# Kernel tuning notes

Hardware: AMD Instinct MI355X
Metric: run time of the kernel (lower is better)

The kernel has to match this reference:

```python
import jax, jax.numpy as jnp
import numpy as np

HEADS = 12
DIM_HEAD = 64
SCALE = DIM_HEAD ** -0.5


def _attn(q, k, v):
    # q: [B, I, D], k/v: [B, J, D]
    sim = jnp.einsum('bid,bjd->bij', q, k)
    a = jax.nn.softmax(sim, axis=-1)
    out = jnp.einsum('bij,bjd->bid', a, v)
    return out, a


def setup_inputs() -> dict:
    key = jax.random.key(0)
    k1, k2, k3 = jax.random.split(key, 3)
    B, F, N, DIM = 8, 8, 196, 768
    x = jax.random.normal(k1, (B, 1 + F * N, DIM), dtype=jnp.float32)
    W_qkv = jax.random.normal(k2, (DIM, 3 * HEADS * DIM_HEAD), dtype=jnp.float32) * (DIM ** -0.5)
    W_out = jax.random.normal(k3, (HEADS * DIM_HEAD, DIM), dtype=jnp.float32) * ((HEADS * DIM_HEAD) ** -0.5)
    b_out = jnp.zeros((DIM,), dtype=jnp.float32)
    return {"x": x, "W_qkv": W_qkv, "W_out": W_out, "b_out": b_out, "f": F}


def reference(x, W_qkv, W_out, b_out, f):
    b, n_tot, dim = x.shape
    h, d = HEADS, DIM_HEAD
    qkv = x @ W_qkv                              # [b, n, 3*h*d]
    q, k, v = jnp.split(qkv, 3, axis=-1)
    # 'b n (h d) -> (b h) n d'
    def to_bh(t):
        return t.reshape(b, n_tot, h, d).transpose(0, 2, 1, 3).reshape(b * h, n_tot, d)
    q, k, v = map(to_bh, (q, k, v))
    q = q * SCALE
    cls_q, q_ = q[:, :1], q[:, 1:]
    cls_k, k_ = k[:, :1], k[:, 1:]
    cls_v, v_ = v[:, :1], v[:, 1:]
    # cls token attends over full sequence
    cls_out, cls_attn = _attn(cls_q, k, v)       # [(b h), 1, d], [(b h), 1, n_tot]
    # spatial attention: 'b (f n) d -> (b f) n d'
    bh = b * h
    n = (n_tot - 1) // f
    def to_bf(t):
        return t.reshape(bh, f, n, d).reshape(bh * f, n, d)
    q_, k_, v_ = map(to_bf, (q_, k_, v_))
    r = f  # q_.shape[0] // cls_k.shape[0]
    # repeat 'b () d -> (b r) () d'
    cls_k_r = jnp.repeat(cls_k, r, axis=0)       # [(bh f), 1, d]
    cls_v_r = jnp.repeat(cls_v, r, axis=0)
    k_ = jnp.concatenate((cls_k_r, k_), axis=1)  # [(bh f), 1+n, d]
    v_ = jnp.concatenate((cls_v_r, v_), axis=1)
    out, _ = _attn(q_, k_, v_)                   # [(bh f), n, d]
    # '(b f) n d -> b (f n) d' (with b := bh)
    out = out.reshape(bh, f * n, d)
    out = jnp.concatenate((cls_out, out), axis=1)  # [(b h), n_tot, d]
    # '(b h) n d -> b n (h d)'
    out = out.reshape(b, h, n_tot, d).transpose(0, 2, 1, 3).reshape(b, n_tot, h * d)
    return out @ W_out + b_out, cls_attn
```

## Files before the change

### kernel.cpp

```cpp
#include <hip/hip_runtime.h>

typedef unsigned short u16;
typedef unsigned int u32;
typedef __attribute__((ext_vector_type(8))) short s16x8;
typedef __attribute__((ext_vector_type(4))) float f32x4;
typedef __attribute__((ext_vector_type(4))) u32 u32x4;
typedef __attribute__((ext_vector_type(4))) float fvec4;

#define DEV static __device__ __forceinline__

typedef __attribute__((address_space(1))) unsigned char ga_u8;
typedef __attribute__((address_space(3))) unsigned char la_u8;

DEV u16 f2bf(float f){
  u32 u = __builtin_bit_cast(u32, f);
  u32 r = (u + 0x7FFFu + ((u >> 16) & 1u)) >> 16;
  return (u16)r;
}
DEV float bf2f(u16 v){
  u32 x = ((u32)v) << 16;
  return __builtin_bit_cast(float, x);
}
DEV f32x4 mfma16(s16x8 a, s16x8 b, f32x4 c){
  return __builtin_amdgcn_mfma_f32_16x16x32_bf16(a, b, c, 0, 0, 0);
}
DEV s16x8 ld16B(const u16* p){
  return __builtin_bit_cast(s16x8, *(const u32x4*)p);
}
DEV u32 cvt_pk_bf16(float lo, float hi){
  u32 r;
  asm volatile("v_cvt_pk_bf16_f32 %0, %1, %2" : "=v"(r) : "v"(lo), "v"(hi));
  return r;
}
DEV void gload16(const void* g, void* l){
  __builtin_amdgcn_global_load_lds((const ga_u8*)g, (la_u8*)l, 16, 0, 0);
}
DEV int xcd_chunk(int bid, int nwg){
  int q = nwg >> 3, r = nwg & 7;
  int xcd = bid & 7, lin = bid >> 3;
  return (xcd < r ? xcd*(q+1) : r*(q+1) + (xcd-r)*q) + lin;
}

#define BARRIER() __builtin_amdgcn_s_barrier()
#define VMC4()    asm volatile("s_waitcnt vmcnt(4)" ::: "memory")
#define VMC0()    asm volatile("s_waitcnt vmcnt(0)" ::: "memory")


__global__ __launch_bounds__(256) void k_prep(const float* __restrict__ x, u16* __restrict__ xb,
                                              const float* __restrict__ Wqkv, u16* __restrict__ wqkvT,
                                              const float* __restrict__ Wout, u16* __restrict__ woutT){
  __shared__ float tile[32][33];
  int b = blockIdx.x, tid = threadIdx.x;
  if (b < 2048){
    const int n4 = 12552*768/4;
    for (int i = b*256 + tid; i < n4; i += 2048*256){
      fvec4 v = ((const fvec4*)x)[i];
      u32 lo = (u32)f2bf(v[0]) | ((u32)f2bf(v[1]) << 16);
      u32 hi = (u32)f2bf(v[2]) | ((u32)f2bf(v[3]) << 16);
      ((u32*)xb)[2*i]   = lo;
      ((u32*)xb)[2*i+1] = hi;
    }
    return;
  }
  const float* W; u16* WT; int K, N, bn, bk;
  if (b < 2048 + 1728){
    int bb = b - 2048; W = Wqkv; WT = wqkvT; K = 768; N = 2304;
    bn = (bb % 72) * 32; bk = (bb / 72) * 32;
  } else {
    int bb = b - 3776; W = Wout; WT = woutT; K = 768; N = 768;
    bn = (bb % 24) * 32; bk = (bb / 24) * 32;
  }
  int tx = tid & 31, ty = tid >> 5;
  #pragma unroll
  for (int r = ty; r < 32; r += 8)
    tile[r][tx] = W[(size_t)(bk + r)*N + bn + tx];
  __syncthreads();
  #pragma unroll
  for (int r = ty; r < 32; r += 8)
    WT[(size_t)(bn + r)*K + bk + tx] = f2bf(tile[tx][r]);
}

__global__ __launch_bounds__(512, 2) void gemm_qkv(const u16* __restrict__ A, const u16* __restrict__ BT,
                                                   u16* __restrict__ qout, u16* __restrict__ kout, u16* __restrict__ vout){
  __shared__ u16 sA[2][2][128*64];
  __shared__ u16 sB[2][2][128*64];
  const int M = 12552;
  const int NWG = 50*9;
  int logical = xcd_chunk(blockIdx.x, NWG);
  int bxi = logical % 9, byi = logical / 9;
  int bm = byi * 256, bn = bxi * 256;

  int tid = threadIdx.x;
  int w = tid >> 6, l = tid & 63, l15 = l & 15, l4 = l >> 4;
  int wm = w >> 2, wn = w & 3;
  int swz = (l15 & 7) << 3;

  f32x4 acc[8][4];
  #pragma unroll
  for (int a=0;a<8;a++)
    #pragma unroll
    for (int b=0;b<4;b++) acc[a][b] = (f32x4){0.f,0.f,0.f,0.f};

  auto stageA = [&](int dbuf, int h, int kt){
    #pragma unroll
    for (int i=0;i<2;i++){
      int ci = i*512 + tid;
      int cs = ci ^ ((ci>>3)&7);
      int r = cs>>3, cc = (cs&7)*8;
      int gr = bm + h*128 + r; if (gr >= M) gr = M-1;
      gload16(A + (size_t)gr*768 + kt*64 + cc, &sA[dbuf][h][(i*512 + (w<<6))*8]);
    }
  };
  auto stageB = [&](int dbuf, int h, int kt){
    #pragma unroll
    for (int i=0;i<2;i++){
      int ci = i*512 + tid;
      int cs = ci ^ ((ci>>3)&7);
      int r = cs>>3, cc = (cs&7)*8;
      gload16(BT + (size_t)(bn + h*128 + r)*768 + kt*64 + cc, &sB[dbuf][h][(i*512 + (w<<6))*8]);
    }
  };

  s16x8 af[4][2], bf[4][2];
  #define LDA_(d, mi, kk) ld16B(&sA[d][wm][(((mi)*16 + l15)*64 + (kk)*32 + l4*8) ^ swz])
  #define LDB_(d, ni, kk) ld16B(&sB[d][(wn*64 + (ni)*16 + l15)>>7][((((wn*64 + (ni)*16 + l15)&127))*64 + (kk)*32 + l4*8) ^ swz])
  #define QUAD(MH, NH) do{ \
    __builtin_amdgcn_s_setprio(1); \
    _Pragma("unroll") \
    for (int j=0;j<4;j++){ \
      _Pragma("unroll") \
      for (int n=0;n<2;n++){ \
        acc[(MH)*4+j][(NH)*2+n] = mfma16(af[j][0], bf[(NH)*2+n][0], acc[(MH)*4+j][(NH)*2+n]); \
        acc[(MH)*4+j][(NH)*2+n] = mfma16(af[j][1], bf[(NH)*2+n][1], acc[(MH)*4+j][(NH)*2+n]); \
      } } \
    __builtin_amdgcn_s_setprio(0); }while(0)

  stageA(0,0,0); stageA(0,1,0); stageB(0,0,0); stageB(0,1,0);
  stageA(1,0,1); stageA(1,1,1);
  VMC4();
  BARRIER();

  #pragma unroll 1
  for (int it = 0; it < 6; ++it){
    int kt1 = 2*it + 1;
    bool full = (it < 5);
    #pragma unroll
    for (int j=0;j<4;j++){ af[j][0]=LDA_(0,j,0); af[j][1]=LDA_(0,j,1); }
    #pragma unroll
    for (int n=0;n<2;n++){ bf[n][0]=LDB_(0,n,0); bf[n][1]=LDB_(0,n,1); }
    stageB(1, 0, kt1);
    BARRIER();
    QUAD(0,0);
    BARRIER();
    #pragma unroll
    for (int n=2;n<4;n++){ bf[n][0]=LDB_(0,n,0); bf[n][1]=LDB_(0,n,1); }
    stageB(1, 1, kt1);
    BARRIER();
    QUAD(0,1);
    BARRIER();
    #pragma unroll
    for (int j=0;j<4;j++){ af[j][0]=LDA_(0,4+j,0); af[j][1]=LDA_(0,4+j,1); }
    if (full){ stageA(0, 0, kt1+1); stageA(0, 1, kt1+1); }
    BARRIER();
    QUAD(1,0); QUAD(1,1);
    if (full) { VMC4(); } else { VMC0(); }
    BARRIER();
    #pragma unroll
    for (int j=0;j<4;j++){ af[j][0]=LDA_(1,j,0); af[j][1]=LDA_(1,j,1); }
    #pragma unroll
    for (int n=0;n<2;n++){ bf[n][0]=LDB_(1,n,0); bf[n][1]=LDB_(1,n,1); }
    if (full) stageB(0, 0, kt1+1);
    BARRIER();
    QUAD(0,0);
    BARRIER();
    #pragma unroll
    for (int n=2;n<4;n++){ bf[n][0]=LDB_(1,n,0); bf[n][1]=LDB_(1,n,1); }
    if (full) stageB(0, 1, kt1+1);
    BARRIER();
    QUAD(0,1);
    BARRIER();
    #pragma unroll
    for (int j=0;j<4;j++){ af[j][0]=LDA_(1,4+j,0); af[j][1]=LDA_(1,4+j,1); }
    if (full){ stageA(1, 0, kt1+2); stageA(1, 1, kt1+2); }
    BARRIER();
    QUAD(1,0); QUAD(1,1);
    if (full) VMC4();
    BARRIER();
  }
  #undef LDA_
  #undef LDB_
  #undef QUAD

  int which = bn / 768;
  int h = ((bn - which*768) >> 6) + wn;
  u16* dst  = (which==0) ? qout : ((which==1) ? kout : vout);
  float scale = (which==0) ? 0.125f : 1.f;
  #pragma unroll
  for (int mi=0; mi<8; mi++){
    #pragma unroll
    for (int r=0; r<4; r++){
      int m = bm + wm*128 + mi*16 + l4*4 + r;
      if (m >= M) continue;
      int b = m / 1569, t = m - b*1569;
      u16* drow = dst + ((size_t)(b*12 + h)*1569 + t)*64 + l15;
      #pragma unroll
      for (int n=0; n<4; n++)
        drow[n*16] = f2bf(acc[mi][n][r] * scale);
    }
  }
}

__global__ __launch_bounds__(256, 2) void k_attn(const u16* __restrict__ qb, const u16* __restrict__ kb,
                                                 const u16* __restrict__ vb, u16* __restrict__ ob,
                                                 float* __restrict__ simw, float* __restrict__ bsum,
                                                 float* __restrict__ pvp){
  __shared__ u16 Vt[64][232];
  __shared__ float rs_lds[4][64];

  int blk = blockIdx.x, tid = threadIdx.x;

  if (blk >= 768){
    int bb = blk - 768;
    int c = bb % 7, g = bb / 7;
    __shared__ float qv[64];
    __shared__ float e_lds[256];
    __shared__ float red[256];
    if (tid < 64) qv[tid] = bf2f(qb[(size_t)g*1569*64 + tid]);
    __syncthreads();
    int j = c*256 + tid;
    float e = 0.f;
    if (j < 1569){
      const u16* kr = kb + ((size_t)g*1569 + j)*64;
      float a = 0.f;
      #pragma unroll
      for (int d0 = 0; d0 < 64; d0 += 8){
        u32x4 u = *(const u32x4*)(kr + d0);
        const u16* us = (const u16*)&u;
        #pragma unroll
        for (int i=0;i<8;i++) a += qv[d0+i]*bf2f(us[i]);
      }
      e = __expf(a - 8.f);
      simw[(size_t)g*1569 + j] = e;
    }
    e_lds[tid] = e;
    red[tid] = e; __syncthreads();
    for (int st=128; st>0; st>>=1){ if (tid<st) red[tid] += red[tid+st]; __syncthreads(); }
    if (tid == 0) bsum[g*8 + c] = red[0];
    int d = tid & 63, kk = tid >> 6;
    float a = 0.f;
    for (int jj = kk; jj < 256; jj += 4){
      int jg = c*256 + jj;
      if (jg < 1569) a += e_lds[jj] * bf2f(vb[((size_t)g*1569+jg)*64 + d]);
    }
    red[tid] = a; __syncthreads();
    if (tid < 64) pvp[((size_t)g*7 + c)*64 + tid] = red[tid]+red[tid+64]+red[tid+128]+red[tid+192];
    return;
  }

  int g = blk;
  int bh = g >> 3, fi = g & 7;
  int w = tid >> 6, l = tid & 63;
  int l15 = l & 15, l4 = l >> 4;

  const u16* qg = qb + ((size_t)bh*1569 + 1 + fi*196)*64;
  const u16* kg = kb + (size_t)bh*1569*64;
  const u16* vg = vb + (size_t)bh*1569*64;

  {
    int jj = tid >> 3, c = (tid & 7)*8, k8 = tid & 7;
    #pragma unroll
    for (int base = 0; base < 224; base += 32){
      int j = base + jj;
      u32x4 vv = {0,0,0,0};
      if (j < 197){
        int t = (j == 0) ? 0 : (1 + fi*196 + j - 1);
        vv = *(const u32x4*)(vg + (size_t)t*64 + c);
      }
      int jl = j & 31;
      int col = (j & ~31) + ((jl>>2)&3)*8 + (jl>>4)*4 + (jl&3);
      const u16* vp = (const u16*)&vv;
      #pragma unroll
      for (int i=0;i<8;i++){ int ii = (i + k8) & 7; Vt[c+ii][col] = vp[ii]; }
    }
  }

  s16x8 qf[4][2];
  #pragma unroll
  for (int mt=0; mt<4; mt++){
    int row = w*64 + mt*16 + l15;
    #pragma unroll
    for (int kk=0; kk<2; kk++){
      if (row < 196) qf[mt][kk] = ld16B(qg + (size_t)row*64 + kk*32 + l4*8);
      else { u32x4 z = {0,0,0,0}; qf[mt][kk] = __builtin_bit_cast(s16x8, z); }
    }
  }

  f32x4 acc[4][4];
  float rsum[4] = {0.f, 0.f, 0.f, 0.f};
  #pragma unroll
  for (int a=0;a<4;a++)
    #pragma unroll
    for (int b=0;b<4;b++) acc[a][b] = (f32x4){0.f,0.f,0.f,0.f};

  __syncthreads();

  #pragma unroll
  for (int ck = 0; ck < 7; ck++){
    int r0 = ck*32 + l15;
    int r1 = r0 + 16;
    int c0 = (r0 < 197 ? r0 : 196);
    int c1 = (r1 < 197 ? r1 : 196);
    int t0 = (r0 == 0) ? 0 : (1 + fi*196 + c0 - 1);
    int t1 = 1 + fi*196 + c1 - 1;
    s16x8 kf0[2], kf1[2];
    #pragma unroll
    for (int kk=0; kk<2; kk++){
      kf0[kk] = ld16B(kg + (size_t)t0*64 + kk*32 + l4*8);
      kf1[kk] = ld16B(kg + (size_t)t1*64 + kk*32 + l4*8);
    }
    s16x8 vf[4];
    #pragma unroll
    for (int ntd=0; ntd<4; ntd++) vf[ntd] = ld16B(&Vt[ntd*16 + l15][ck*32 + l4*8]);
    int kbase = ck*32 + l4*4;

    #pragma unroll
    for (int mt=0; mt<4; mt++){
      __builtin_amdgcn_s_setprio(1);
      f32x4 s0 = (f32x4){0.f,0.f,0.f,0.f}, s1 = (f32x4){0.f,0.f,0.f,0.f};
      s0 = mfma16(kf0[0], qf[mt][0], s0);
      s0 = mfma16(kf0[1], qf[mt][1], s0);
      s1 = mfma16(kf1[0], qf[mt][0], s1);
      s1 = mfma16(kf1[1], qf[mt][1], s1);
      __builtin_amdgcn_s_setprio(0);
      float p[8];
      #pragma unroll
      for (int r=0; r<4; r++){
        p[r]   = (kbase + r      < 197) ? __expf(s0[r] - 8.f) : 0.f;
        p[4+r] = (kbase + 16 + r < 197) ? __expf(s1[r] - 8.f) : 0.f;
      }
      rsum[mt] += ((p[0]+p[1])+(p[2]+p[3])) + ((p[4]+p[5])+(p[6]+p[7]));
      u32x4 pw;
      pw[0] = cvt_pk_bf16(p[0], p[1]);
      pw[1] = cvt_pk_bf16(p[2], p[3]);
      pw[2] = cvt_pk_bf16(p[4], p[5]);
      pw[3] = cvt_pk_bf16(p[6], p[7]);
      s16x8 pa = __builtin_bit_cast(s16x8, pw);
      __builtin_amdgcn_s_setprio(1);
      #pragma unroll
      for (int ntd=0; ntd<4; ntd++)
        acc[mt][ntd] = mfma16(pa, vf[ntd], acc[mt][ntd]);
      __builtin_amdgcn_s_setprio(0);
    }
  }

  #pragma unroll
  for (int mt=0; mt<4; mt++){
    float rs = rsum[mt];
    rs += __shfl_xor(rs, 16);
    rs += __shfl_xor(rs, 32);
    rs_lds[w][mt*16 + l15] = rs;
  }

  u16* og = ob + ((size_t)bh*1569 + 1 + fi*196)*64;
  #pragma unroll
  for (int mt=0; mt<4; mt++){
    #pragma unroll
    for (int r=0; r<4; r++){
      int row = w*64 + mt*16 + l4*4 + r;
      if (row < 196){
        float inv = 1.f / rs_lds[w][mt*16 + l4*4 + r];
        #pragma unroll
        for (int ntd=0; ntd<4; ntd++)
          og[(size_t)row*64 + ntd*16 + l15] = f2bf(acc[mt][ntd][r] * inv);
      }
    }
  }
}

__global__ __launch_bounds__(256) void cls_b(const float* __restrict__ simw, const float* __restrict__ bsum,
                                             const float* __restrict__ pvp, float* __restrict__ attn,
                                             u16* __restrict__ ob){
  int g = blockIdx.x, tid = threadIdx.x;
  float s = 0.f;
  #pragma unroll
  for (int c=0;c<7;c++) s += bsum[g*8+c];
  float inv = 1.f/s;
  for (int j = tid; j < 1569; j += 256)
    attn[(size_t)g*1569+j] = simw[(size_t)g*1569+j]*inv;
  if (tid < 64){
    float a = 0.f;
    #pragma unroll
    for (int c=0;c<7;c++) a += pvp[((size_t)g*7+c)*64 + tid];
    ob[(size_t)g*1569*64 + tid] = f2bf(a*inv);
  }
}

__global__ __launch_bounds__(512, 2) void gemm_out(const u16* __restrict__ AO, const u16* __restrict__ BT,
                                                   const float* __restrict__ bias, float* __restrict__ C){
  __shared__ u16 sA[2][2][128*64];
  __shared__ u16 sB[2][2][128*64];
  const int M = 12552;
  const int NWG = 50*3;
  int logical = xcd_chunk(blockIdx.x, NWG);
  int bxi = logical % 3, byi = logical / 3;
  int bm = byi * 256, bn = bxi * 256;

  int tid = threadIdx.x;
  int w = tid >> 6, l = tid & 63, l15 = l & 15, l4 = l >> 4;
  int wm = w >> 2, wn = w & 3;
  int swz = (l15 & 7) << 3;

  f32x4 acc[8][4];
  #pragma unroll
  for (int a=0;a<8;a++)
    #pragma unroll
    for (int b=0;b<4;b++) acc[a][b] = (f32x4){0.f,0.f,0.f,0.f};

  auto stageA = [&](int dbuf, int h, int kt){
    #pragma unroll
    for (int i=0;i<2;i++){
      int ci = i*512 + tid;
      int cs = ci ^ ((ci>>3)&7);
      int r = cs>>3, cc = (cs&7)*8;
      int gr = bm + h*128 + r; if (gr >= M) gr = M-1;
      int b = gr / 1569, t = gr - b*1569;
      gload16(AO + ((size_t)(b*12 + kt)*1569 + t)*64 + cc, &sA[dbuf][h][(i*512 + (w<<6))*8]);
    }
  };
  auto stageB = [&](int dbuf, int h, int kt){
    #pragma unroll
    for (int i=0;i<2;i++){
      int ci = i*512 + tid;
      int cs = ci ^ ((ci>>3)&7);
      int r = cs>>3, cc = (cs&7)*8;
      gload16(BT + (size_t)(bn + h*128 + r)*768 + kt*64 + cc, &sB[dbuf][h][(i*512 + (w<<6))*8]);
    }
  };

  s16x8 af[4][2], bf[4][2];
  #define LDA_(d, mi, kk) ld16B(&sA[d][wm][(((mi)*16 + l15)*64 + (kk)*32 + l4*8) ^ swz])
  #define LDB_(d, ni, kk) ld16B(&sB[d][(wn*64 + (ni)*16 + l15)>>7][((((wn*64 + (ni)*16 + l15)&127))*64 + (kk)*32 + l4*8) ^ swz])
  #define QUAD(MH, NH) do{ \
    __builtin_amdgcn_s_setprio(1); \
    _Pragma("unroll") \
    for (int j=0;j<4;j++){ \
      _Pragma("unroll") \
      for (int n=0;n<2;n++){ \
        acc[(MH)*4+j][(NH)*2+n] = mfma16(af[j][0], bf[(NH)*2+n][0], acc[(MH)*4+j][(NH)*2+n]); \
        acc[(MH)*4+j][(NH)*2+n] = mfma16(af[j][1], bf[(NH)*2+n][1], acc[(MH)*4+j][(NH)*2+n]); \
      } } \
    __builtin_amdgcn_s_setprio(0); }while(0)

  stageA(0,0,0); stageA(0,1,0); stageB(0,0,0); stageB(0,1,0);
  stageA(1,0,1); stageA(1,1,1);
  VMC4();
  BARRIER();

  #pragma unroll 1
  for (int it = 0; it < 6; ++it){
    int kt1 = 2*it + 1;
    bool full = (it < 5);
    #pragma unroll
    for (int j=0;j<4;j++){ af[j][0]=LDA_(0,j,0); af[j][1]=LDA_(0,j,1); }
    #pragma unroll
    for (int n=0;n<2;n++){ bf[n][0]=LDB_(0,n,0); bf[n][1]=LDB_(0,n,1); }
    stageB(1, 0, kt1);
    BARRIER();
    QUAD(0,0);
    BARRIER();
    #pragma unroll
    for (int n=2;n<4;n++){ bf[n][0]=LDB_(0,n,0); bf[n][1]=LDB_(0,n,1); }
    stageB(1, 1, kt1);
    BARRIER();
    QUAD(0,1);
    BARRIER();
    #pragma unroll
    for (int j=0;j<4;j++){ af[j][0]=LDA_(0,4+j,0); af[j][1]=LDA_(0,4+j,1); }
    if (full){ stageA(0, 0, kt1+1); stageA(0, 1, kt1+1); }
    BARRIER();
    QUAD(1,0); QUAD(1,1);
    if (full) { VMC4(); } else { VMC0(); }
    BARRIER();
    #pragma unroll
    for (int j=0;j<4;j++){ af[j][0]=LDA_(1,j,0); af[j][1]=LDA_(1,j,1); }
    #pragma unroll
    for (int n=0;n<2;n++){ bf[n][0]=LDB_(1,n,0); bf[n][1]=LDB_(1,n,1); }
    if (full) stageB(0, 0, kt1+1);
    BARRIER();
    QUAD(0,0);
    BARRIER();
    #pragma unroll
    for (int n=2;n<4;n++){ bf[n][0]=LDB_(1,n,0); bf[n][1]=LDB_(1,n,1); }
    if (full) stageB(0, 1, kt1+1);
    BARRIER();
    QUAD(0,1);
    BARRIER();
    #pragma unroll
    for (int j=0;j<4;j++){ af[j][0]=LDA_(1,4+j,0); af[j][1]=LDA_(1,4+j,1); }
    if (full){ stageA(1, 0, kt1+2); stageA(1, 1, kt1+2); }
    BARRIER();
    QUAD(1,0); QUAD(1,1);
    if (full) VMC4();
    BARRIER();
  }
  #undef LDA_
  #undef LDB_
  #undef QUAD

  int n0 = bn + wn*64;
  float bv[4];
  #pragma unroll
  for (int n=0;n<4;n++) bv[n] = bias[n0 + n*16 + l15];
  #pragma unroll
  for (int mi=0; mi<8; mi++){
    #pragma unroll
    for (int r=0; r<4; r++){
      int m = bm + wm*128 + mi*16 + l4*4 + r;
      if (m >= M) continue;
      float* crow = C + (size_t)m*768 + n0 + l15;
      #pragma unroll
      for (int n=0; n<4; n++)
        crow[n*16] = acc[mi][n][r] + bv[n];
    }
  }
}

extern "C" void kernel_launch(void* const* d_in, const int* in_sizes, int n_in,
                              void* d_out, int out_size, void* d_ws, size_t ws_size,
                              hipStream_t stream){
  (void)in_sizes; (void)n_in; (void)out_size;
  const float* x    = (const float*)d_in[0];
  const float* Wqkv = (const float*)d_in[1];
  const float* Wout = (const float*)d_in[2];
  const float* bout = (const float*)d_in[3];
  float* out0 = (float*)d_out;
  float* out1 = out0 + (size_t)12552*768;

  char* ws = (char*)d_ws;
  size_t off = 0;
  auto alloc = [&](size_t bytes)->char*{
    char* p = ws + off;
    off += (bytes + 255) & ~(size_t)255;
    return p;
  };
  u16* xb    = (u16*)alloc((size_t)12552*768*2);
  u16* wqkvT = (u16*)alloc((size_t)2304*768*2);
  u16* woutT = (u16*)alloc((size_t)768*768*2);
  u16* qb    = (u16*)alloc((size_t)96*1569*64*2);
  u16* kbuf  = (u16*)alloc((size_t)96*1569*64*2);
  u16* vbuf  = (u16*)alloc((size_t)96*1569*64*2);
  u16* ao    = (u16*)alloc((size_t)96*1569*64*2);
  float* simw = (float*)alloc((size_t)96*1569*4);
  float* bsum = (float*)alloc((size_t)96*8*4);
  float* pvp  = (float*)alloc((size_t)96*7*64*4);
  if (off > ws_size) return;

  k_prep<<<4352, 256, 0, stream>>>(x, xb, Wqkv, wqkvT, Wout, woutT);
  gemm_qkv<<<50*9, 512, 0, stream>>>(xb, wqkvT, qb, kbuf, vbuf);
  k_attn<<<1440, 256, 0, stream>>>(qb, kbuf, vbuf, ao, simw, bsum, pvp);
  cls_b<<<96, 256, 0, stream>>>(simw, bsum, pvp, out1, ao);
  gemm_out<<<50*3, 512, 0, stream>>>(ao, woutT, bout, out0);
}
```

Baseline: 170.0 us.

## Split cls attention into its own kernel and software-pipeline QK MFMAs

The fused attention kernel is split into two launches: cls_a, which computes the cls-token partial softmax and PV, and k_frame, which handles per-frame spatial attention. Separating them lets each kernel get its own register and LDS allocation, so the frame kernel no longer carries the cls branch's shared arrays and code. Inside the frame loop, the QK MFMAs for the next m-tile are issued before the exp/pack of the current tile, so matrix work overlaps the transcendental math. The inline asm for bf16 packing also drops volatile to let the compiler schedule it. The costs are an extra kernel launch, a serialization point between the two kernels, and higher register pressure from the prefetched score tiles.

```diff
diff --git a/kernel.cpp b/kernel.cpp
--- a/kernel.cpp
+++ b/kernel.cpp
@@ -29,7 +29,7 @@
 }
 DEV u32 cvt_pk_bf16(float lo, float hi){
   u32 r;
-  asm volatile("v_cvt_pk_bf16_f32 %0, %1, %2" : "=v"(r) : "v"(lo), "v"(hi));
+  asm("v_cvt_pk_bf16_f32 %0, %1, %2" : "=v"(r) : "v"(lo), "v"(hi));
   return r;
 }
 DEV void gload16(const void* g, void* l){
@@ -210,54 +210,52 @@
   }
 }
 
-__global__ __launch_bounds__(256, 2) void k_attn(const u16* __restrict__ qb, const u16* __restrict__ kb,
-                                                 const u16* __restrict__ vb, u16* __restrict__ ob,
-                                                 float* __restrict__ simw, float* __restrict__ bsum,
-                                                 float* __restrict__ pvp){
+__global__ __launch_bounds__(256) void cls_a(const u16* __restrict__ qb, const u16* __restrict__ kb,
+                                             const u16* __restrict__ vb, float* __restrict__ simw,
+                                             float* __restrict__ bsum, float* __restrict__ pvp){
+  int bb = blockIdx.x;
+  int c = bb % 7, g = bb / 7;
+  int tid = threadIdx.x;
+  __shared__ float qv[64];
+  __shared__ float e_lds[256];
+  __shared__ float red[256];
+  if (tid < 64) qv[tid] = bf2f(qb[(size_t)g*1569*64 + tid]);
+  __syncthreads();
+  int j = c*256 + tid;
+  float e = 0.f;
+  if (j < 1569){
+    const u16* kr = kb + ((size_t)g*1569 + j)*64;
+    float a = 0.f;
+    #pragma unroll
+    for (int d0 = 0; d0 < 64; d0 += 8){
+      u32x4 u = *(const u32x4*)(kr + d0);
+      const u16* us = (const u16*)&u;
+      #pragma unroll
+      for (int i=0;i<8;i++) a += qv[d0+i]*bf2f(us[i]);
+    }
+    e = __expf(a - 8.f);
+    simw[(size_t)g*1569 + j] = e;
+  }
+  e_lds[tid] = e;
+  red[tid] = e; __syncthreads();
+  for (int st=128; st>0; st>>=1){ if (tid<st) red[tid] += red[tid+st]; __syncthreads(); }
+  if (tid == 0) bsum[g*8 + c] = red[0];
+  int d = tid & 63, kk = tid >> 6;
+  float a = 0.f;
+  for (int jj = kk; jj < 256; jj += 4){
+    int jg = c*256 + jj;
+    if (jg < 1569) a += e_lds[jj] * bf2f(vb[((size_t)g*1569+jg)*64 + d]);
+  }
+  red[tid] = a; __syncthreads();
+  if (tid < 64) pvp[((size_t)g*7 + c)*64 + tid] = red[tid]+red[tid+64]+red[tid+128]+red[tid+192];
+}
+
+__global__ __launch_bounds__(256, 2) void k_frame(const u16* __restrict__ qb, const u16* __restrict__ kb,
+                                                  const u16* __restrict__ vb, u16* __restrict__ ob){
   __shared__ u16 Vt[64][232];
   __shared__ float rs_lds[4][64];
 
-  int blk = blockIdx.x, tid = threadIdx.x;
-
-  if (blk >= 768){
-    int bb = blk - 768;
-    int c = bb % 7, g = bb / 7;
-    __shared__ float qv[64];
-    __shared__ float e_lds[256];
-    __shared__ float red[256];
-    if (tid < 64) qv[tid] = bf2f(qb[(size_t)g*1569*64 + tid]);
-    __syncthreads();
-    int j = c*256 + tid;
-    float e = 0.f;
-    if (j < 1569){
-      const u16* kr = kb + ((size_t)g*1569 + j)*64;
-      float a = 0.f;
-      #pragma unroll
-      for (int d0 = 0; d0 < 64; d0 += 8){
-        u32x4 u = *(const u32x4*)(kr + d0);
-        const u16* us = (const u16*)&u;
-        #pragma unroll
-        for (int i=0;i<8;i++) a += qv[d0+i]*bf2f(us[i]);
-      }
-      e = __expf(a - 8.f);
-      simw[(size_t)g*1569 + j] = e;
-    }
-    e_lds[tid] = e;
-    red[tid] = e; __syncthreads();
-    for (int st=128; st>0; st>>=1){ if (tid<st) red[tid] += red[tid+st]; __syncthreads(); }
-    if (tid == 0) bsum[g*8 + c] = red[0];
-    int d = tid & 63, kk = tid >> 6;
-    float a = 0.f;
-    for (int jj = kk; jj < 256; jj += 4){
-      int jg = c*256 + jj;
-      if (jg < 1569) a += e_lds[jj] * bf2f(vb[((size_t)g*1569+jg)*64 + d]);
-    }
-    red[tid] = a; __syncthreads();
-    if (tid < 64) pvp[((size_t)g*7 + c)*64 + tid] = red[tid]+red[tid+64]+red[tid+128]+red[tid+192];
-    return;
-  }
-
-  int g = blk;
+  int g = blockIdx.x, tid = threadIdx.x;
   int bh = g >> 3, fi = g & 7;
   int w = tid >> 6, l = tid & 63;
   int l15 = l & 15, l4 = l >> 4;
@@ -323,20 +321,25 @@
     for (int ntd=0; ntd<4; ntd++) vf[ntd] = ld16B(&Vt[ntd*16 + l15][ck*32 + l4*8]);
     int kbase = ck*32 + l4*4;
 
+    #define QKPAIR(m, d0, d1) do{ \
+      __builtin_amdgcn_s_setprio(1); \
+      d0 = (f32x4){0.f,0.f,0.f,0.f}; d1 = (f32x4){0.f,0.f,0.f,0.f}; \
+      d0 = mfma16(kf0[0], qf[m][0], d0); \
+      d0 = mfma16(kf0[1], qf[m][1], d0); \
+      d1 = mfma16(kf1[0], qf[m][0], d1); \
+      d1 = mfma16(kf1[1], qf[m][1], d1); \
+      __builtin_amdgcn_s_setprio(0); }while(0)
+
+    f32x4 sc0, sc1, nx0, nx1;
+    QKPAIR(0, sc0, sc1);
     #pragma unroll
     for (int mt=0; mt<4; mt++){
-      __builtin_amdgcn_s_setprio(1);
-      f32x4 s0 = (f32x4){0.f,0.f,0.f,0.f}, s1 = (f32x4){0.f,0.f,0.f,0.f};
-      s0 = mfma16(kf0[0], qf[mt][0], s0);
-      s0 = mfma16(kf0[1], qf[mt][1], s0);
-      s1 = mfma16(kf1[0], qf[mt][0], s1);
-      s1 = mfma16(kf1[1], qf[mt][1], s1);
-      __builtin_amdgcn_s_setprio(0);
+      if (mt < 3) QKPAIR(mt+1, nx0, nx1);
       float p[8];
       #pragma unroll
       for (int r=0; r<4; r++){
-        p[r]   = (kbase + r      < 197) ? __expf(s0[r] - 8.f) : 0.f;
-        p[4+r] = (kbase + 16 + r < 197) ? __expf(s1[r] - 8.f) : 0.f;
+        p[r]   = (kbase + r      < 197) ? __expf(sc0[r] - 8.f) : 0.f;
+        p[4+r] = (kbase + 16 + r < 197) ? __expf(sc1[r] - 8.f) : 0.f;
       }
       rsum[mt] += ((p[0]+p[1])+(p[2]+p[3])) + ((p[4]+p[5])+(p[6]+p[7]));
       u32x4 pw;
@@ -350,7 +353,9 @@
       for (int ntd=0; ntd<4; ntd++)
         acc[mt][ntd] = mfma16(pa, vf[ntd], acc[mt][ntd]);
       __builtin_amdgcn_s_setprio(0);
-    }
+      sc0 = nx0; sc1 = nx1;
+    }
+    #undef QKPAIR
   }
 
   #pragma unroll
@@ -557,7 +562,8 @@
 
   k_prep<<<4352, 256, 0, stream>>>(x, xb, Wqkv, wqkvT, Wout, woutT);
   gemm_qkv<<<50*9, 512, 0, stream>>>(xb, wqkvT, qb, kbuf, vbuf);
-  k_attn<<<1440, 256, 0, stream>>>(qb, kbuf, vbuf, ao, simw, bsum, pvp);
+  cls_a<<<672, 256, 0, stream>>>(qb, kbuf, vbuf, simw, bsum, pvp);
+  k_frame<<<768, 256, 0, stream>>>(qb, kbuf, vbuf, ao);
   cls_b<<<96, 256, 0, stream>>>(simw, bsum, pvp, out1, ao);
   gemm_out<<<50*3, 512, 0, stream>>>(ao, woutT, bout, out0);
 }
```

Result: no change. 168.7 us (-0.7%).
